# Kernel tuning notes

Hardware: AMD Instinct MI355X
Metric: run time of the kernel (lower is better)

The kernel has to match this reference:

```python
import jax, jax.numpy as jnp
import numpy as np

N = 10000      # nodes
E = 1_000_000  # edges (avg degree 100)
T = 6          # time steps (states.size(0)); T-1 recurrent steps
HID = 32       # hidden_feats, forced by M out=32 and U in=2*hid


def _linear(key, fan_in, fan_out):
    k1, k2 = jax.random.split(key)
    s = 1.0 / np.sqrt(fan_in)
    w = jax.random.uniform(k1, (fan_in, fan_out), minval=-s, maxval=s, dtype=jnp.float32)
    b = jax.random.uniform(k2, (fan_out,), minval=-s, maxval=s, dtype=jnp.float32)
    return w, b


def setup_inputs() -> dict:
    key = jax.random.key(0)
    ks = jax.random.split(key, 12)
    states = jax.random.normal(ks[0], (T, N), dtype=jnp.float32)
    priority = jax.random.uniform(ks[1], (N,), dtype=jnp.float32)
    edges_mat = jax.random.normal(ks[2], (N, N), dtype=jnp.float32) * 0.1
    src = jax.random.randint(ks[3], (E,), 0, N)
    # dst constructed so every node has at least one incoming edge (segment_max well-defined)
    dst = jnp.arange(E, dtype=jnp.int32) % N
    enc_w, enc_b = _linear(ks[4], 1 + HID + 1, HID)   # encoder: in_feats + hidden + 1
    M_w, M_b = _linear(ks[5], 2 * HID + 1, HID)        # M: 2*hidden + edge_feats -> 32
    U_w, U_b = _linear(ks[6], 2 * HID, HID)
    dn_w, dn_b = _linear(ks[7], 2 * HID, 1)            # decoder_nextnode
    du_w, du_b = _linear(ks[8], 2 * HID + 1, 1)        # decoder_update
    term_w, term_b = _linear(ks[9], HID, 1)
    return dict(states=states, priority=priority, edges_mat=edges_mat, src=src, dst=dst,
                enc_w=enc_w, enc_b=enc_b, M_w=M_w, M_b=M_b, U_w=U_w, U_b=U_b,
                dn_w=dn_w, dn_b=dn_b, du_w=du_w, du_b=du_b, term_w=term_w, term_b=term_b)


def reference(states, priority, edges_mat, src, dst,
              enc_w, enc_b, M_w, M_b, U_w, U_b,
              dn_w, dn_b, du_w, du_b, term_w, term_b):
    n = states.shape[1]
    t = states.shape[0]
    edge_feat = edges_mat[src, dst]  # (E,) gather like edges_mat[graph.edges()]
    pri = priority[:, None]          # (N,1)

    def step(carry, _):
        state, hidden = carry                                   # (N,), (N,HID)
        inp = jnp.concatenate([state[:, None], hidden, pri], 1)  # (N, 1+HID+1)
        z = inp @ enc_w + enc_b                                  # (N, HID)
        m_in = jnp.concatenate([z[src], z[dst], edge_feat[:, None]], 1)  # (E, 2*HID+1)
        msg = m_in @ M_w + M_b                                   # (E, HID)
        u_input = jax.ops.segment_max(msg, dst, num_segments=n)  # max-reduce into dst mailboxes
        new_hidden = jnp.concatenate([z, u_input], 1) @ U_w + U_b  # (N, HID)
        h_mean = jnp.mean(new_hidden, axis=0, keepdims=True)
        loc = jnp.concatenate([new_hidden, h_mean], 0) @ term_w + term_b  # (N+1, 1)
        stop = jnp.max(jax.nn.sigmoid(loc))
        nne = jnp.concatenate([new_hidden, z], 1) @ dn_w + dn_b   # (N,1)
        new_state = (jnp.concatenate([new_hidden, z, nne], 1) @ du_w + du_b)[:, 0]  # (N,)
        return (new_state, new_hidden), (new_state, stop, nne[:, 0])

    hidden0 = jnp.zeros((n, HID), dtype=states.dtype)
    _, (new_states, stops, nnes) = jax.lax.scan(step, (states[0], hidden0), None, length=t - 1)

    preds = jnp.concatenate([states[0:1], new_states], 0)                 # (T, N)
    preds_stop = jnp.concatenate([jnp.zeros((1,), preds.dtype), stops])[None, :, None]  # (1, T, 1)
    preds_nextnode = nnes.T[:, :, None]                                   # (N, T-1, 1)
    return preds, preds_stop, preds_nextnode
```

## Files before the change

### kernel.cpp

```cpp
#include <hip/hip_runtime.h>
#include <hip/hip_cooperative_groups.h>
#include <math.h>

namespace cg = cooperative_groups;

#define NN 10000
#define EE 1000000
#define HIDN 32
#define NSTEP 5
#define GROUPS 8
#define NBLK (NN / GROUPS)
#define NTHR 256

#define STOP_OFF (6*NN)
#define PN_OFF   (6*NN + 6)

__device__ __forceinline__ unsigned fkey(float f) {
  unsigned u = __float_as_uint(f);
  return (u & 0x80000000u) ? ~u : (u | 0x80000000u);
}
__device__ __forceinline__ float fkey_dec(unsigned k) {
  unsigned u = (k & 0x80000000u) ? (k ^ 0x80000000u) : ~k;
  return __uint_as_float(u);
}

__global__ __launch_bounds__(NTHR, 5) void k_all(
    const float* __restrict__ states, const float* __restrict__ pri,
    const float* __restrict__ edges_mat, const int* __restrict__ src,
    const float* __restrict__ enc_w, const float* __restrict__ enc_b,
    const float* __restrict__ M_w, const float* __restrict__ M_b,
    const float* __restrict__ U_w, const float* __restrict__ U_b,
    const float* __restrict__ dn_w, const float* __restrict__ dn_b,
    const float* __restrict__ du_w, const float* __restrict__ du_b,
    const float* __restrict__ term_w, const float* __restrict__ term_b,
    int2* __restrict__ se, float* __restrict__ Abuf,
    float* __restrict__ parth,
    float* __restrict__ partm,
    float* __restrict__ d_out)
{
  __shared__ float s_ew[34 * 32];
  __shared__ float s_ms[1024], s_md[1024], s_uwz[1024], s_uwu[1024];
  __shared__ float s_eb[32], s_mb[32], s_ub[32];
  __shared__ float s_zr[GROUPS][32], s_ur[GROUPS][32], s_nh[GROUPS][32];
  __shared__ float s_loc[GROUPS];
  __shared__ float s_red[GROUPS][32];
  __shared__ float s_redm[4];

  const int tid = threadIdx.x;
  const int g = tid >> 5, o = tid & 31;
  const int j = blockIdx.x * GROUPS + g;
  const int gid = blockIdx.x * NTHR + tid;

  for (int e = gid; e < EE; e += NBLK * NTHR) {
    int s = src[e];
    int d = e % NN;
    float ef = edges_mat[(size_t)s * NN + d];
    se[e] = make_int2(s, __float_as_int(ef));
  }
  for (int x = gid; x < NN; x += NBLK * NTHR) d_out[x] = states[x];
  if (gid == 0) d_out[STOP_OFF] = 0.f;

  for (int i = tid; i < 34 * 32; i += NTHR) s_ew[i] = enc_w[i];
  for (int i = tid; i < 1024; i += NTHR) {
    s_ms[i]  = M_w[i];        s_md[i]  = M_w[1024 + i];
    s_uwz[i] = U_w[i];        s_uwu[i] = U_w[1024 + i];
  }
  if (tid < 32) { s_eb[tid] = enc_b[tid]; s_mb[tid] = M_b[tid]; s_ub[tid] = U_b[tid]; }
  __syncthreads();

  const float pr   = pri[j];
  const float mw64 = M_w[64 * 32 + o];
  const float twv  = term_w[o];
  const float dnw0 = dn_w[o], dnw1 = dn_w[32 + o];
  const float duw0 = du_w[o], duw1 = du_w[32 + o];
  const float du64 = du_w[64], dnb0 = dn_b[0], dub0 = du_b[0];
  const float tb0  = term_b[0];

  float z_reg, base_reg;
  {
    float st = states[j];
    float zv = s_eb[o] + st * s_ew[o] + pr * s_ew[33 * 32 + o];
    s_zr[g][o] = zv;
    __syncthreads();
    float av = 0.f, bv = s_mb[o];
    #pragma unroll
    for (int i = 0; i < 32; i++) {
      float zi = s_zr[g][i];
      av = fmaf(zi, s_ms[i * 32 + o], av);
      bv = fmaf(zi, s_md[i * 32 + o], bv);
    }
    Abuf[(j << 5) | o] = av;
    z_reg = zv; base_reg = bv;
  }

  cg::grid_group grid = cg::this_grid();
  grid.sync();

  for (int t = 0; t < NSTEP; t++) {
    if (blockIdx.x == 0 && t > 0) {
      const int pb = (t - 1) & 1;
      float acc = 0.f;
      for (int b = g; b < NBLK; b += GROUPS)
        acc += parth[(size_t)pb * NBLK * 32 + b * 32 + o];
      float mxv = -3.4e38f;
      for (int b = tid; b < NBLK; b += NTHR)
        mxv = fmaxf(mxv, partm[pb * NBLK + b]);
      #pragma unroll
      for (int m = 32; m >= 1; m >>= 1) mxv = fmaxf(mxv, __shfl_xor(mxv, m, 64));
      if ((tid & 63) == 0) s_redm[tid >> 6] = mxv;
      s_red[g][o] = acc;
      __syncthreads();
      if (tid < 32) {
        float tot = 0.f;
        #pragma unroll
        for (int gg = 0; gg < GROUPS; gg++) tot += s_red[gg][tid];
        float v = tot * (1.0f / NN) * twv;
        #pragma unroll
        for (int m = 16; m >= 1; m >>= 1) v += __shfl_xor(v, m, 32);
        if (tid == 0) {
          float mall = fmaxf(fmaxf(s_redm[0], s_redm[1]), fmaxf(s_redm[2], s_redm[3]));
          float mx = fmaxf(mall, v);
          d_out[STOP_OFF + t] = 1.f / (1.f + expf(-(mx + tb0)));
        }
      }
    }

    const float* __restrict__ Ar = Abuf + (size_t)(t & 1) * (NN * HIDN);
    float red0 = -3.4e38f, red1 = -3.4e38f;
    {
      const int2* sep = se + j;
      #pragma unroll 2
      for (int kb = 0; kb < 100; kb += 10) {
        int2 v[10];
        #pragma unroll
        for (int q = 0; q < 10; q++) v[q] = sep[(kb + q) * NN];
        #pragma unroll
        for (int q = 0; q < 10; q++) {
          float a = Ar[(v[q].x << 5) | o];
          float m = fmaf(__int_as_float(v[q].y), mw64, a);
          if (q & 1) red1 = fmaxf(red1, m); else red0 = fmaxf(red0, m);
        }
      }
    }
    float u_o = fmaxf(red0, red1) + base_reg;

    s_zr[g][o] = z_reg; s_ur[g][o] = u_o;
    __syncthreads();
    float nh = s_ub[o];
    #pragma unroll
    for (int i = 0; i < 32; i++) {
      nh = fmaf(s_zr[g][i], s_uwz[i * 32 + o], nh);
      nh = fmaf(s_ur[g][i], s_uwu[i * 32 + o], nh);
    }

    float lv  = nh * twv;
    float dnv = nh * dnw0 + z_reg * dnw1;
    float duv = nh * duw0 + z_reg * duw1;
    #pragma unroll
    for (int m = 16; m >= 1; m >>= 1) {
      lv  += __shfl_xor(lv,  m, 32);
      dnv += __shfl_xor(dnv, m, 32);
      duv += __shfl_xor(duv, m, 32);
    }
    float nne = dnv + dnb0;
    float ns  = duv + nne * du64 + dub0;
    if (o == 0) {
      d_out[(t + 1) * NN + j]       = ns;
      d_out[PN_OFF + j * NSTEP + t] = nne;
      s_loc[g] = lv;
    }
    s_nh[g][o] = nh;
    __syncthreads();

    if (tid < 32) {
      float hp = 0.f;
      #pragma unroll
      for (int gg = 0; gg < GROUPS; gg++) hp += s_nh[gg][tid];
      parth[(size_t)(t & 1) * NBLK * 32 + blockIdx.x * 32 + tid] = hp;
    }
    if (tid == 0) {
      float m = s_loc[0];
      #pragma unroll
      for (int gg = 1; gg < GROUPS; gg++) m = fmaxf(m, s_loc[gg]);
      partm[(t & 1) * NBLK + blockIdx.x] = m;
    }

    if (t < NSTEP - 1) {
      float z2 = s_eb[o] + ns * s_ew[o] + pr * s_ew[33 * 32 + o];
      #pragma unroll
      for (int i = 0; i < 32; i++) z2 = fmaf(s_nh[g][i], s_ew[(1 + i) * 32 + o], z2);
      __syncthreads();
      s_zr[g][o] = z2;
      __syncthreads();
      float av2 = 0.f, bv2 = s_mb[o];
      #pragma unroll
      for (int i = 0; i < 32; i++) {
        float zi = s_zr[g][i];
        av2 = fmaf(zi, s_ms[i * 32 + o], av2);
        bv2 = fmaf(zi, s_md[i * 32 + o], bv2);
      }
      float* __restrict__ Aw = Abuf + (size_t)((t + 1) & 1) * (NN * HIDN);
      Aw[(j << 5) | o] = av2;
      z_reg = z2; base_reg = bv2;
    }

    grid.sync();
  }

  if (blockIdx.x == 0) {
    float acc = 0.f;
    for (int b = g; b < NBLK; b += GROUPS)
      acc += parth[(size_t)0 * NBLK * 32 + b * 32 + o];
    float mxv = -3.4e38f;
    for (int b = tid; b < NBLK; b += NTHR)
      mxv = fmaxf(mxv, partm[b]);
    #pragma unroll
    for (int m = 32; m >= 1; m >>= 1) mxv = fmaxf(mxv, __shfl_xor(mxv, m, 64));
    if ((tid & 63) == 0) s_redm[tid >> 6] = mxv;
    s_red[g][o] = acc;
    __syncthreads();
    if (tid < 32) {
      float tot = 0.f;
      #pragma unroll
      for (int gg = 0; gg < GROUPS; gg++) tot += s_red[gg][tid];
      float v = tot * (1.0f / NN) * twv;
      #pragma unroll
      for (int m = 16; m >= 1; m >>= 1) v += __shfl_xor(v, m, 32);
      if (tid == 0) {
        float mall = fmaxf(fmaxf(s_redm[0], s_redm[1]), fmaxf(s_redm[2], s_redm[3]));
        float mx = fmaxf(mall, v);
        d_out[STOP_OFF + NSTEP] = 1.f / (1.f + expf(-(mx + tb0)));
      }
    }
  }
}

__global__ __launch_bounds__(256) void k_pre(
    const int* __restrict__ src,
    const float* __restrict__ edges_mat, const float* __restrict__ states,
    int2* __restrict__ se, float* __restrict__ hidden, float* __restrict__ d_out,
    float* __restrict__ hsum, unsigned* __restrict__ locmax)
{
  int i = blockIdx.x * blockDim.x + threadIdx.x;
  int stride = blockDim.x * gridDim.x;
  for (int e = i; e < EE; e += stride) {
    int s = src[e];
    int d = e % NN;
    float ef = edges_mat[(size_t)s * NN + d];
    se[e] = make_int2(s, __float_as_int(ef));
  }
  for (int x = i; x < NN * HIDN; x += stride) hidden[x] = 0.f;
  for (int x = i; x < NN; x += stride) d_out[x] = states[x];
  if (i == 0) { d_out[STOP_OFF] = 0.f; *locmax = 0u; }
  if (i >= 256 && i < 256 + 32) hsum[i - 256] = 0.f;
}

__global__ __launch_bounds__(256) void k_znode(
    const float* __restrict__ state, const float* __restrict__ pri,
    const float* __restrict__ hidden,
    const float* __restrict__ enc_w, const float* __restrict__ enc_b,
    const float* __restrict__ M_w, const float* __restrict__ M_b,
    const float* __restrict__ term_w, const float* __restrict__ term_b,
    float* __restrict__ z, float* __restrict__ A, float* __restrict__ base,
    float* __restrict__ hsum, unsigned* __restrict__ locmax,
    float* __restrict__ d_out, int t)
{
  __shared__ float s_ew[34 * 32], s_eb[32], s_ms[32 * 32], s_md[32 * 32], s_mb[32];
  __shared__ float s_h[GROUPS][32], s_z[GROUPS][32];
  int tid = threadIdx.x;
  for (int i = tid; i < 34 * 32; i += 256) s_ew[i] = enc_w[i];
  for (int i = tid; i < 32 * 32; i += 256) { s_ms[i] = M_w[i]; s_md[i] = M_w[32 * 32 + i]; }
  if (tid < 32) { s_eb[tid] = enc_b[tid]; s_mb[tid] = M_b[tid]; }

  if (blockIdx.x == 0 && t > 0 && tid < 32) {
    float v = hsum[tid] * (1.0f / NN) * term_w[tid];
    #pragma unroll
    for (int m = 16; m >= 1; m >>= 1) v += __shfl_xor(v, m, 32);
    if (tid == 0) {
      float mx = fmaxf(fkey_dec(*locmax), v);
      d_out[STOP_OFF + t] = 1.f / (1.f + expf(-(mx + term_b[0])));
      *locmax = 0u;
    }
    hsum[tid] = 0.f;
  }

  int g = tid >> 5, o = tid & 31;
  int j = blockIdx.x * GROUPS + g;
  s_h[g][o] = hidden[(j << 5) | o];
  __syncthreads();
  float st = state[j], pr = pri[j];
  float zv = s_eb[o] + st * s_ew[o] + pr * s_ew[33 * 32 + o];
  #pragma unroll
  for (int i = 0; i < 32; i++) zv = fmaf(s_h[g][i], s_ew[(1 + i) * 32 + o], zv);
  s_z[g][o] = zv;
  z[(j << 5) | o] = zv;
  __syncthreads();
  float av = 0.f, bv = s_mb[o];
  #pragma unroll
  for (int i = 0; i < 32; i++) {
    float zi = s_z[g][i];
    av = fmaf(zi, s_ms[i * 32 + o], av);
    bv = fmaf(zi, s_md[i * 32 + o], bv);
  }
  A[(j << 5) | o] = av;
  base[(j << 5) | o] = bv;
}

__global__ __launch_bounds__(256) void k_edge(
    const int2* __restrict__ se,
    const float* __restrict__ z, const float* __restrict__ A,
    const float* __restrict__ base,
    const float* __restrict__ U_w, const float* __restrict__ U_b,
    const float* __restrict__ dn_w, const float* __restrict__ dn_b,
    const float* __restrict__ du_w, const float* __restrict__ du_b,
    const float* __restrict__ term_w, const float* __restrict__ M_w,
    float* __restrict__ hidden, float* __restrict__ d_out,
    float* __restrict__ hsum, unsigned* __restrict__ locmax, int t)
{
  __shared__ float s_uwz[32 * 32], s_uwu[32 * 32], s_ub[32];
  __shared__ float s_zr[GROUPS][32], s_ur[GROUPS][32], s_nh[GROUPS][32];
  __shared__ float s_loc[GROUPS];
  int tid = threadIdx.x;
  for (int i = tid; i < 32 * 32; i += 256) { s_uwz[i] = U_w[i]; s_uwu[i] = U_w[32 * 32 + i]; }
  if (tid < 32) s_ub[tid] = U_b[tid];
  int g = tid >> 5, o = tid & 31;
  int j = blockIdx.x * GROUPS + g;
  float mw64 = M_w[64 * 32 + o];

  float red = -3.4e38f;
  #pragma unroll 4
  for (int k = 0; k < 100; k++) {
    int2 v = se[j + k * NN];
    float a = A[(v.x << 5) | o];
    red = fmaxf(red, fmaf(__int_as_float(v.y), mw64, a));
  }
  float u_o = red + base[(j << 5) | o];
  float z_o = z[(j << 5) | o];
  s_zr[g][o] = z_o; s_ur[g][o] = u_o;
  __syncthreads();
  float nh = s_ub[o];
  #pragma unroll
  for (int i = 0; i < 32; i++) {
    nh = fmaf(s_zr[g][i], s_uwz[i * 32 + o], nh);
    nh = fmaf(s_ur[g][i], s_uwu[i * 32 + o], nh);
  }
  hidden[(j << 5) | o] = nh;

  float lv  = nh * term_w[o];
  float dnv = nh * dn_w[o] + z_o * dn_w[32 + o];
  float duv = nh * du_w[o] + z_o * du_w[32 + o];
  #pragma unroll
  for (int m = 16; m >= 1; m >>= 1) {
    lv  += __shfl_xor(lv,  m, 32);
    dnv += __shfl_xor(dnv, m, 32);
    duv += __shfl_xor(duv, m, 32);
  }
  if (o == 0) {
    float nne = dnv + dn_b[0];
    float nsv = duv + nne * du_w[64] + du_b[0];
    d_out[(t + 1) * NN + j] = nsv;
    d_out[PN_OFF + j * NSTEP + t] = nne;
    s_loc[g] = lv;
  }
  s_nh[g][o] = nh;
  __syncthreads();
  if (tid < 32) {
    float hp = 0.f;
    #pragma unroll
    for (int gg = 0; gg < GROUPS; gg++) hp += s_nh[gg][tid];
    atomicAdd(&hsum[tid], hp);
  }
  if (tid == 0) {
    float m = s_loc[0];
    #pragma unroll
    for (int gg = 1; gg < GROUPS; gg++) m = fmaxf(m, s_loc[gg]);
    atomicMax(locmax, fkey(m));
  }
}

__global__ void k_stop(const float* __restrict__ hsum, const unsigned* __restrict__ locmax,
                       const float* __restrict__ term_w, const float* __restrict__ term_b,
                       float* __restrict__ d_out, int t)
{
  int o = threadIdx.x;
  float v = (o < 32) ? (hsum[o] * (1.0f / NN)) * term_w[o] : 0.f;
  #pragma unroll
  for (int m = 16; m >= 1; m >>= 1) v += __shfl_xor(v, m, 32);
  if (o == 0) {
    float mx = fmaxf(fkey_dec(*locmax), v);
    float x = mx + term_b[0];
    d_out[STOP_OFF + 1 + t] = 1.f / (1.f + expf(-x));
  }
}

extern "C" void kernel_launch(void* const* d_in, const int* in_sizes, int n_in,
                              void* d_out_v, int out_size, void* d_ws, size_t ws_size,
                              hipStream_t stream)
{
  const float* states = (const float*)d_in[0];
  const float* pri    = (const float*)d_in[1];
  const float* edges  = (const float*)d_in[2];
  const int*   src    = (const int*)d_in[3];
  const float* enc_w  = (const float*)d_in[5];
  const float* enc_b  = (const float*)d_in[6];
  const float* M_w    = (const float*)d_in[7];
  const float* M_b    = (const float*)d_in[8];
  const float* U_w    = (const float*)d_in[9];
  const float* U_b    = (const float*)d_in[10];
  const float* dn_w   = (const float*)d_in[11];
  const float* dn_b   = (const float*)d_in[12];
  const float* du_w   = (const float*)d_in[13];
  const float* du_b   = (const float*)d_in[14];
  const float* term_w = (const float*)d_in[15];
  const float* term_b = (const float*)d_in[16];
  float* out = (float*)d_out_v;
  float* ws = (float*)d_ws;

  static int coop_ok = -1;
  if (coop_ok < 0) {
    int nb = 0;
    hipError_t e1 = hipOccupancyMaxActiveBlocksPerMultiprocessor(&nb, k_all, NTHR, 0);
    hipDeviceProp_t prop;
    int dev = 0;
    hipGetDevice(&dev);
    hipError_t e2 = hipGetDeviceProperties(&prop, dev);
    coop_ok = (e1 == hipSuccess && e2 == hipSuccess &&
               prop.cooperativeLaunch &&
               (long)nb * prop.multiProcessorCount >= NBLK) ? 1 : 0;
  }

  if (coop_ok == 1) {
    int2*  se     = (int2*)ws;
    float* Abuf   = ws + 2 * EE;
    float* parth  = Abuf + 2 * NN * HIDN;
    float* partm  = parth + 2 * NBLK * 32;

    void* args[] = {
      (void*)&states, (void*)&pri, (void*)&edges, (void*)&src,
      (void*)&enc_w, (void*)&enc_b, (void*)&M_w, (void*)&M_b,
      (void*)&U_w, (void*)&U_b, (void*)&dn_w, (void*)&dn_b,
      (void*)&du_w, (void*)&du_b, (void*)&term_w, (void*)&term_b,
      (void*)&se, (void*)&Abuf, (void*)&parth, (void*)&partm, (void*)&out
    };
    hipLaunchCooperativeKernel((void*)k_all, dim3(NBLK), dim3(NTHR), args, 0, stream);
    return;
  }

  int2*  se     = (int2*)ws;
  float* z      = ws + 2 * EE;
  float* Abuf   = z + NN * HIDN;
  float* base   = Abuf + NN * HIDN;
  float* hidden = base + NN * HIDN;
  float* hsum   = hidden + NN * HIDN;
  unsigned* locmax = (unsigned*)(hsum + 32);

  hipLaunchKernelGGL(k_pre, dim3(4096), dim3(256), 0, stream,
                     src, edges, states, se, hidden, out, hsum, locmax);
  for (int t = 0; t < NSTEP; t++) {
    const float* state = out + t * NN;
    hipLaunchKernelGGL(k_znode, dim3(NN / GROUPS), dim3(256), 0, stream,
                       state, pri, hidden, enc_w, enc_b, M_w, M_b, term_w, term_b,
                       z, Abuf, base, hsum, locmax, out, t);
    hipLaunchKernelGGL(k_edge, dim3(NN / GROUPS), dim3(256), 0, stream,
                       se, z, Abuf, base, U_w, U_b, dn_w, dn_b, du_w, du_b,
                       term_w, M_w, hidden, out, hsum, locmax, t);
  }
  hipLaunchKernelGGL(k_stop, dim3(1), dim3(64), 0, stream,
                     hsum, locmax, term_w, term_b, out, NSTEP - 1);
}
```

Before: 799.1 us.

## Keep per-block edge sources and features in shared memory instead of global se buffer

```diff
diff --git a/kernel.cpp b/kernel.cpp
--- a/kernel.cpp
+++ b/kernel.cpp
@@ -11,6 +11,7 @@
 #define GROUPS 8
 #define NBLK (NN / GROUPS)
 #define NTHR 256
+#define DEG 100
 
 #define STOP_OFF (6*NN)
 #define PN_OFF   (6*NN + 6)
@@ -33,7 +34,7 @@
     const float* __restrict__ dn_w, const float* __restrict__ dn_b,
     const float* __restrict__ du_w, const float* __restrict__ du_b,
     const float* __restrict__ term_w, const float* __restrict__ term_b,
-    int2* __restrict__ se, float* __restrict__ Abuf,
+    float* __restrict__ Abuf,
     float* __restrict__ parth,
     float* __restrict__ partm,
     float* __restrict__ d_out)
@@ -45,17 +46,26 @@
   __shared__ float s_loc[GROUPS];
   __shared__ float s_red[GROUPS][32];
   __shared__ float s_redm[4];
+  __shared__ int   s_so[GROUPS][DEG];
+  __shared__ float s_ef[GROUPS][DEG];
 
   const int tid = threadIdx.x;
   const int g = tid >> 5, o = tid & 31;
-  const int j = blockIdx.x * GROUPS + g;
+  const int jbase = blockIdx.x * GROUPS;
+  const int j = jbase + g;
   const int gid = blockIdx.x * NTHR + tid;
 
-  for (int e = gid; e < EE; e += NBLK * NTHR) {
-    int s = src[e];
-    int d = e % NN;
-    float ef = edges_mat[(size_t)s * NN + d];
-    se[e] = make_int2(s, __float_as_int(ef));
+  #pragma unroll
+  for (int i = 0; i < 4; i++) {
+    int idx = tid + i * NTHR;
+    if (idx < GROUPS * DEG) {
+      int gg = idx & 7, kk = idx >> 3;
+      int e = jbase + gg + kk * NN;
+      int s = src[e];
+      float ef = edges_mat[(size_t)s * NN + jbase + gg];
+      s_so[gg][kk] = s << 5;
+      s_ef[gg][kk] = ef;
+    }
   }
   for (int x = gid; x < NN; x += NBLK * NTHR) d_out[x] = states[x];
   if (gid == 0) d_out[STOP_OFF] = 0.f;
@@ -127,19 +137,17 @@
 
     const float* __restrict__ Ar = Abuf + (size_t)(t & 1) * (NN * HIDN);
     float red0 = -3.4e38f, red1 = -3.4e38f;
-    {
-      const int2* sep = se + j;
-      #pragma unroll 2
-      for (int kb = 0; kb < 100; kb += 10) {
-        int2 v[10];
-        #pragma unroll
-        for (int q = 0; q < 10; q++) v[q] = sep[(kb + q) * NN];
-        #pragma unroll
-        for (int q = 0; q < 10; q++) {
-          float a = Ar[(v[q].x << 5) | o];
-          float m = fmaf(__int_as_float(v[q].y), mw64, a);
-          if (q & 1) red1 = fmaxf(red1, m); else red0 = fmaxf(red0, m);
-        }
+    #pragma unroll 1
+    for (int kb = 0; kb < DEG; kb += 20) {
+      int off[20]; float av[20];
+      #pragma unroll
+      for (int q = 0; q < 20; q++) off[q] = s_so[g][kb + q] | o;
+      #pragma unroll
+      for (int q = 0; q < 20; q++) av[q] = Ar[off[q]];
+      #pragma unroll
+      for (int q = 0; q < 20; q++) {
+        float m = fmaf(s_ef[g][kb + q], mw64, av[q]);
+        if (q & 1) red1 = fmaxf(red1, m); else red0 = fmaxf(red0, m);
       }
     }
     float u_o = fmaxf(red0, red1) + base_reg;
@@ -430,8 +438,7 @@
   }
 
   if (coop_ok == 1) {
-    int2*  se     = (int2*)ws;
-    float* Abuf   = ws + 2 * EE;
+    float* Abuf   = ws;
     float* parth  = Abuf + 2 * NN * HIDN;
     float* partm  = parth + 2 * NBLK * 32;
 
@@ -440,7 +447,7 @@
       (void*)&enc_w, (void*)&enc_b, (void*)&M_w, (void*)&M_b,
       (void*)&U_w, (void*)&U_b, (void*)&dn_w, (void*)&dn_b,
       (void*)&du_w, (void*)&du_b, (void*)&term_w, (void*)&term_b,
-      (void*)&se, (void*)&Abuf, (void*)&parth, (void*)&partm, (void*)&out
+      (void*)&Abuf, (void*)&parth, (void*)&partm, (void*)&out
     };
     hipLaunchCooperativeKernel((void*)k_all, dim3(NBLK), dim3(NTHR), args, 0, stream);
     return;
```

Measured after the change: 798.1 us. About the same (-0.1%).
